# Optimization experiments

Hardware: AMD Instinct MI355X
Metric: run time of the kernel (lower is better)

Reference implementation:

```python
import jax, jax.numpy as jnp
import numpy as np

DIM = 128
CODEBOOK_SIZE = 1024
DECAY = 0.99
EPSILON = 1e-06


def setup_inputs() -> dict:
    key = jax.random.key(0)
    k1, k2, k3, k4 = jax.random.split(key, 4)
    x = jax.random.normal(k1, (64, 1024, DIM), dtype=jnp.float32)
    embed = jax.random.normal(k2, (CODEBOOK_SIZE, DIM), dtype=jnp.float32)
    # keep all codes above the dead-code threshold (2) so expire_codes_ is a no-op
    cluster_size = jax.random.uniform(k3, (CODEBOOK_SIZE,), dtype=jnp.float32) * 10.0 + 2.0
    embed_avg = jax.random.normal(k4, (CODEBOOK_SIZE, DIM), dtype=jnp.float32)
    return {"x": x, "embed": embed, "cluster_size": cluster_size, "embed_avg": embed_avg}


def reference(x, embed, cluster_size, embed_avg):
    shape = x.shape
    xf = x.reshape(-1, shape[-1])  # [N, D]

    # quantize: squared euclidean distances [N, K] then argmin
    dist = (
        jnp.sum(xf * xf, axis=1, keepdims=True)
        - 2.0 * (xf @ embed.T)
        + jnp.sum(embed * embed, axis=1)[None, :]
    )
    embed_ind_flat = jnp.argmin(dist, axis=-1)  # [N]
    embed_ind = embed_ind_flat.reshape(shape[:-1])

    # dequantize
    quantize = embed[embed_ind]  # [..., D]

    # training EMA updates (one-hot scatter accumulation)
    one_hot_sum = jax.ops.segment_sum(
        jnp.ones_like(embed_ind_flat, dtype=x.dtype), embed_ind_flat,
        num_segments=CODEBOOK_SIZE)
    embed_sum = jax.ops.segment_sum(xf, embed_ind_flat, num_segments=CODEBOOK_SIZE)  # [K, D]

    cluster_size_new = cluster_size * DECAY + one_hot_sum * (1.0 - DECAY)
    embed_avg_new = embed_avg * DECAY + embed_sum * (1.0 - DECAY)

    total = jnp.sum(cluster_size_new)
    smoothed = (cluster_size_new + EPSILON) / (total + EPSILON * CODEBOOK_SIZE) * total
    embed_new = embed_avg_new / smoothed[:, None]

    return quantize, embed_ind, cluster_size_new, embed_avg_new, embed_new
```

## Files before the change

kernel.cpp:

```cpp
#include <hip/hip_runtime.h>
#include <hip/hip_fp16.h>
#include <float.h>

#define DIMD   128
#define KCODES 1024
#define NROWS  65536
#define TAU    0.03f
#define SEG_R  16

typedef __attribute__((ext_vector_type(8)))  _Float16 half8;
typedef __attribute__((ext_vector_type(16))) float f32x16;

union U8 { uint4 u; half8 h; };

__device__ __forceinline__ unsigned packh2(float a, float b) {
    __half2 t = __floats2half2_rn(a, b);
    return *(unsigned*)&t;
}

__global__ __launch_bounds__(256) void pre_kernel(
    const float* __restrict__ embed, uint4* __restrict__ ehg,
    float* __restrict__ enorm, uint4* __restrict__ zero_region)
{
    if (blockIdx.x < 64) {
        int t = blockIdx.x * 256 + threadIdx.x;
        int chunk = t >> 9;
        int s = (t >> 6) & 7;
        int L = t & 63;
        const float* src = embed + ((size_t)(chunk * 32 + (L & 31)) * DIMD) + s * 16 + (L >> 5) * 8;
        float4 a = *(const float4*)src;
        float4 b = *(const float4*)(src + 4);
        float f[8] = {a.x, a.y, a.z, a.w, b.x, b.y, b.z, b.w};
        uint4 H;
        unsigned* hw = (unsigned*)&H;
#pragma unroll
        for (int j = 0; j < 4; ++j) hw[j] = packh2(f[2 * j], f[2 * j + 1]);
        ehg[t] = H;
    } else if (blockIdx.x < 68) {
        int k = (blockIdx.x - 64) * 256 + threadIdx.x;
        const float4* e = (const float4*)(embed + (size_t)k * DIMD);
        float s = 0.f;
#pragma unroll
        for (int c = 0; c < DIMD / 4; ++c) {
            float4 v = e[c];
            s += v.x * v.x + v.y * v.y + v.z * v.z + v.w * v.w;
        }
        enorm[k] = s;
    } else {
        uint4 z = {0, 0, 0, 0};
        zero_region[threadIdx.x] = z;
        zero_region[threadIdx.x + 256] = z;
    }
}

__global__ __launch_bounds__(256, 2) void argmin_mfma(
    const float* __restrict__ x, const uint4* __restrict__ ehg,
    const float* __restrict__ enorm,
    int* __restrict__ ind_i, float* __restrict__ ind_f,
    int* __restrict__ wl, int* __restrict__ wl_cnt)
{
    __shared__ uint4 Bs[512];

    const int tid  = threadIdx.x;
    const int wave = tid >> 6;
    const int lane = tid & 63;
    const int n    = lane & 31;
    const int h    = lane >> 5;
    const int row0 = blockIdx.x * 128;
    const int rowA = row0 + wave * 32 + n;

    uint4 xh[8], xl[8];
    const float* xrow = x + (size_t)rowA * DIMD + h * 8;
#pragma unroll
    for (int s = 0; s < 8; ++s) {
        float4 a = *(const float4*)(xrow + s * 16);
        float4 b = *(const float4*)(xrow + s * 16 + 4);
        float f[8] = {a.x, a.y, a.z, a.w, b.x, b.y, b.z, b.w};
        unsigned* ph = (unsigned*)&xh[s];
        unsigned* pl = (unsigned*)&xl[s];
#pragma unroll
        for (int j = 0; j < 4; ++j) {
            float u0 = f[2 * j], u1 = f[2 * j + 1];
            __half2 hh = __floats2half2_rn(u0, u1);
            ph[j] = *(unsigned*)&hh;
            float2 back = __half22float2(hh);
            __half2 ll = __floats2half2_rn(u0 - back.x, u1 - back.y);
            pl[j] = *(unsigned*)&ll;
        }
    }

    float bestv[16], best2[16];
    int   besti[16];
#pragma unroll
    for (int r = 0; r < 16; ++r) { bestv[r] = FLT_MAX; best2[r] = FLT_MAX; besti[r] = 0; }

    for (int chunk = 0; chunk < KCODES / 32; ++chunk) {
        __syncthreads();
        {
            const uint4* sh = ehg + chunk * 512;
            Bs[tid]       = sh[tid];
            Bs[tid + 256] = sh[tid + 256];
        }
        float ee_val = enorm[chunk * 32 + n];
        __syncthreads();

        f32x16 acc;
#pragma unroll
        for (int r = 0; r < 16; ++r) acc[r] = 0.f;

#pragma unroll
        for (int s = 0; s < 8; ++s) {
            U8 ah, al, bh;
            ah.u = xh[s]; al.u = xl[s];
            bh.u = Bs[s * 64 + lane];
            acc = __builtin_amdgcn_mfma_f32_32x32x16_f16(ah.h, bh.h, acc, 0, 0, 0);
            acc = __builtin_amdgcn_mfma_f32_32x32x16_f16(al.h, bh.h, acc, 0, 0, 0);
        }

        const int nglob = chunk * 32 + n;
#pragma unroll
        for (int r = 0; r < 16; ++r) {
            float d = fmaf(-2.f, acc[r], ee_val);
            bool c1 = d < bestv[r];
            float t = c1 ? bestv[r] : d;
            best2[r] = fminf(best2[r], t);
            besti[r] = c1 ? nglob : besti[r];
            bestv[r] = fminf(bestv[r], d);
        }
    }

#pragma unroll
    for (int m = 1; m <= 16; m <<= 1) {
#pragma unroll
        for (int r = 0; r < 16; ++r) {
            float ov = __shfl_xor(bestv[r], m, 64);
            float o2 = __shfl_xor(best2[r], m, 64);
            int   oi = __shfl_xor(besti[r], m, 64);
            float hi = fmaxf(bestv[r], ov);
            best2[r] = fminf(fminf(best2[r], o2), hi);
            bool take = (ov < bestv[r]) || (ov == bestv[r] && oi < besti[r]);
            bestv[r] = take ? ov : bestv[r];
            besti[r] = take ? oi : besti[r];
        }
    }

    if (n == 0) {
#pragma unroll
        for (int r = 0; r < 16; ++r) {
            int row = row0 + wave * 32 + (r & 3) + 8 * (r >> 2) + 4 * h;
            ind_i[row] = besti[r];
            ind_f[row] = (float)besti[r];
            if (best2[r] - bestv[r] < TAU) {
                int p = atomicAdd(wl_cnt, 1);
                if (p < NROWS) wl[p] = row;
            }
        }
    }
}

__global__ __launch_bounds__(256) void recheck_kernel(
    const float* __restrict__ x, const float* __restrict__ embed,
    const float* __restrict__ enorm, const int* __restrict__ wl,
    const int* __restrict__ wl_cnt, int* __restrict__ ind_i, float* __restrict__ ind_f)
{
    __shared__ float xs[DIMD];
    __shared__ float rv[256];
    __shared__ int   ri[256];
    const int tid = threadIdx.x;
    int count = *wl_cnt;
    if (count > NROWS) count = NROWS;

    for (int i = blockIdx.x; i < count; i += gridDim.x) {
        const int row = wl[i];
        __syncthreads();
        if (tid < DIMD) xs[tid] = x[(size_t)row * DIMD + tid];
        __syncthreads();

        const float4* xs4 = (const float4*)xs;
        float xn = 0.f;
#pragma unroll 8
        for (int c = 0; c < 32; ++c) {
            float4 v = xs4[c];
            xn += v.x * v.x + v.y * v.y + v.z * v.z + v.w * v.w;
        }

        float bv = FLT_MAX; int bi = 0;
#pragma unroll
        for (int c = 0; c < 4; ++c) {
            int code = tid * 4 + c;
            const float4* er = (const float4*)(embed + (size_t)code * DIMD);
            float acc = 0.f;
#pragma unroll 8
            for (int kk = 0; kk < 32; ++kk) {
                float4 a = xs4[kk];
                float4 b = er[kk];
                acc += a.x * b.x + a.y * b.y + a.z * b.z + a.w * b.w;
            }
            float d = (xn - 2.0f * acc) + enorm[code];
            if (d < bv) { bv = d; bi = code; }
        }
        rv[tid] = bv; ri[tid] = bi;
        __syncthreads();
        for (int s = 128; s > 0; s >>= 1) {
            if (tid < s) {
                if (rv[tid + s] < rv[tid] || (rv[tid + s] == rv[tid] && ri[tid + s] < ri[tid])) {
                    rv[tid] = rv[tid + s]; ri[tid] = ri[tid + s];
                }
            }
            __syncthreads();
        }
        if (tid == 0) {
            int s_new = ri[0];
            if (s_new != ind_i[row]) {
                ind_i[row] = s_new;
                ind_f[row] = (float)s_new;
            }
        }
        __syncthreads();
    }
}

__global__ __launch_bounds__(256) void hist_kernel(
    const int* __restrict__ ind, int* __restrict__ counts)
{
    __shared__ int hcnt[KCODES];
    for (int i = threadIdx.x; i < KCODES; i += 256) hcnt[i] = 0;
    __syncthreads();
    const int base = blockIdx.x * 2048;
    for (int i = threadIdx.x; i < 2048; i += 256) atomicAdd(&hcnt[ind[base + i]], 1);
    __syncthreads();
    for (int i = threadIdx.x; i < KCODES; i += 256) {
        int v = hcnt[i];
        if (v) atomicAdd(&counts[i], v);
    }
}

__global__ __launch_bounds__(1024) void scan_cluster_kernel(
    const int* __restrict__ counts, const float* __restrict__ cluster_size,
    int* __restrict__ cursor, float* __restrict__ out_cs, float* __restrict__ smoothed)
{
    __shared__ int   s[KCODES];
    __shared__ float rf[KCODES];
    const int t = threadIdx.x;
    int my = counts[t];
    s[t] = my;
    float cs = cluster_size[t] * 0.99f + (float)my * 0.01f;
    out_cs[t] = cs;
    rf[t] = cs;
    __syncthreads();
    for (int d = 1; d < KCODES; d <<= 1) {
        int v = (t >= d) ? s[t - d] : 0;
        __syncthreads();
        s[t] += v;
        __syncthreads();
    }
    cursor[t] = s[t] - my;
    for (int st = 512; st > 0; st >>= 1) {
        if (t < st) rf[t] += rf[t + st];
        __syncthreads();
    }
    float total = rf[0];
    smoothed[t] = (cs + 1e-6f) / (total + 1e-6f * (float)KCODES) * total;
}

__global__ __launch_bounds__(256) void permbuild_kernel(
    const int* __restrict__ ind, int* __restrict__ cursor,
    int* __restrict__ perm, int* __restrict__ codes, uint4* __restrict__ embed_sum4)
{
    const int tid = threadIdx.x;
    if (tid < 128) {
        uint4 z = {0, 0, 0, 0};
        embed_sum4[blockIdx.x * 128 + tid] = z;
    }
    const int row = blockIdx.x * 256 + tid;
    const int k = ind[row];
    int pos = atomicAdd(&cursor[k], 1);
    perm[pos] = row;
    codes[pos] = k;
}

__global__ __launch_bounds__(256) void segsum_kernel(
    const float* __restrict__ x, const float* __restrict__ embed,
    const int* __restrict__ perm, const int* __restrict__ codes,
    float* __restrict__ embed_sum, float* __restrict__ out_q)
{
    const int g = (blockIdx.x * 256 + threadIdx.x) >> 5;
    const int c = threadIdx.x & 31;
    const int base = g * SEG_R;

    float4 acc = {0.f, 0.f, 0.f, 0.f};
    int curk = codes[base];
#pragma unroll
    for (int j = 0; j < SEG_R; ++j) {
        int r = perm[base + j];
        int k = codes[base + j];
        float4 v = *(const float4*)(x + (size_t)r * DIMD + c * 4);
        float4 e = *(const float4*)(embed + (size_t)k * DIMD + c * 4);
        *(float4*)(out_q + (size_t)r * DIMD + c * 4) = e;
        if (k != curk) {
            float* dst = embed_sum + (size_t)curk * DIMD + c * 4;
            atomicAdd(dst + 0, acc.x);
            atomicAdd(dst + 1, acc.y);
            atomicAdd(dst + 2, acc.z);
            atomicAdd(dst + 3, acc.w);
            acc = v;
            curk = k;
        } else {
            acc.x += v.x; acc.y += v.y; acc.z += v.z; acc.w += v.w;
        }
    }
    float* dst = embed_sum + (size_t)curk * DIMD + c * 4;
    atomicAdd(dst + 0, acc.x);
    atomicAdd(dst + 1, acc.y);
    atomicAdd(dst + 2, acc.z);
    atomicAdd(dst + 3, acc.w);
}

__global__ void embed_kernel(
    const float* __restrict__ embed_avg, const float* __restrict__ embed_sum,
    const float* __restrict__ smoothed, float* __restrict__ out_ea,
    float* __restrict__ out_en)
{
    int i = blockIdx.x * blockDim.x + threadIdx.x;
    if (i < KCODES * DIMD) {
        float ea = embed_avg[i] * 0.99f + embed_sum[i] * 0.01f;
        out_ea[i] = ea;
        out_en[i] = ea / smoothed[i >> 7];
    }
}

extern "C" void kernel_launch(void* const* d_in, const int* in_sizes, int n_in,
                              void* d_out, int out_size, void* d_ws, size_t ws_size,
                              hipStream_t stream) {
    const float* x            = (const float*)d_in[0];
    const float* embed        = (const float*)d_in[1];
    const float* cluster_size = (const float*)d_in[2];
    const float* embed_avg    = (const float*)d_in[3];

    float* out     = (float*)d_out;
    float* out_q   = out;
    float* out_ind = out + 8388608;
    float* out_cs  = out + 8454144;
    float* out_ea  = out + 8455168;
    float* out_en  = out + 8586240;

    char* ws = (char*)d_ws;
    int*   ind_i     = (int*)(ws + 0);
    float* enorm     = (float*)(ws + 262144);
    int*   countsI   = (int*)(ws + 266240);
    int*   wl_cnt    = (int*)(ws + 270336);
    int*   cursor    = (int*)(ws + 274432);
    float* smoothed  = (float*)(ws + 278528);
    int*   perm      = (int*)(ws + 286720);
    int*   wl        = (int*)(ws + 548864);
    int*   codes     = (int*)(ws + 548864);
    uint4* ehg       = (uint4*)(ws + 811008);
    float* embed_sum = (float*)(ws + 811008);

    pre_kernel<<<69, 256, 0, stream>>>(embed, ehg, enorm, (uint4*)countsI);
    argmin_mfma<<<NROWS / 128, 256, 0, stream>>>(
        x, ehg, enorm, ind_i, out_ind, wl, wl_cnt);
    recheck_kernel<<<512, 256, 0, stream>>>(
        x, embed, enorm, wl, wl_cnt, ind_i, out_ind);
    hist_kernel<<<32, 256, 0, stream>>>(ind_i, countsI);
    scan_cluster_kernel<<<1, 1024, 0, stream>>>(countsI, cluster_size, cursor, out_cs, smoothed);
    permbuild_kernel<<<NROWS / 256, 256, 0, stream>>>(
        ind_i, cursor, perm, codes, (uint4*)embed_sum);
    segsum_kernel<<<(NROWS / SEG_R) * 32 / 256, 256, 0, stream>>>(
        x, embed, perm, codes, embed_sum, out_q);
    embed_kernel<<<(KCODES * DIMD + 255) / 256, 256, 0, stream>>>(
        embed_avg, embed_sum, smoothed, out_ea, out_en);
}
```

Measured before the change: 240.9 us.

## Double-buffer codebook tiles via direct global-to-LDS loads and pack argmin keys

Codebook chunks are staged into a double-buffered LDS array with global_load_lds, so the next chunk's load overlaps the current chunk's MFMAs and one barrier per iteration is removed. Codebook norms are preloaded into shared memory once per block. The running argmin packs the chunk index into the low mantissa bits of the distance and tracks min and second-min with integer min/max, replacing the float compares and selects. The near-tie threshold is raised slightly to absorb the lost mantissa precision, which sends more rows to recheck. Integer ordering of negative float bit patterns also risks picking the wrong code.

```diff
diff --git a/kernel.cpp b/kernel.cpp
--- a/kernel.cpp
+++ b/kernel.cpp
@@ -5,7 +5,7 @@
 #define DIMD   128
 #define KCODES 1024
 #define NROWS  65536
-#define TAU    0.03f
+#define TAU    0.032f
 #define SEG_R  16
 
 typedef __attribute__((ext_vector_type(8)))  _Float16 half8;
@@ -16,6 +16,12 @@
 __device__ __forceinline__ unsigned packh2(float a, float b) {
     __half2 t = __floats2half2_rn(a, b);
     return *(unsigned*)&t;
+}
+
+__device__ __forceinline__ void stage16(const uint4* g, uint4* l) {
+    auto* gp = (const __attribute__((address_space(1))) uint4*)g;
+    auto* lp = (__attribute__((address_space(3))) uint4*)l;
+    __builtin_amdgcn_global_load_lds(gp, lp, 16, 0, 0);
 }
 
 __global__ __launch_bounds__(256) void pre_kernel(
@@ -59,7 +65,8 @@
     int* __restrict__ ind_i, float* __restrict__ ind_f,
     int* __restrict__ wl, int* __restrict__ wl_cnt)
 {
-    __shared__ uint4 Bs[512];
+    __shared__ uint4 Bs[2][512];
+    __shared__ float Es[KCODES];
 
     const int tid  = threadIdx.x;
     const int wave = tid >> 6;
@@ -69,15 +76,20 @@
     const int row0 = blockIdx.x * 128;
     const int rowA = row0 + wave * 32 + n;
 
-    uint4 xh[8], xl[8];
+    stage16(ehg + tid,       &Bs[0][tid]);
+    stage16(ehg + tid + 256, &Bs[0][tid + 256]);
+    ((float4*)Es)[tid] = ((const float4*)enorm)[tid];
+
+    half8 xh[8], xl[8];
     const float* xrow = x + (size_t)rowA * DIMD + h * 8;
 #pragma unroll
     for (int s = 0; s < 8; ++s) {
         float4 a = *(const float4*)(xrow + s * 16);
         float4 b = *(const float4*)(xrow + s * 16 + 4);
         float f[8] = {a.x, a.y, a.z, a.w, b.x, b.y, b.z, b.w};
-        unsigned* ph = (unsigned*)&xh[s];
-        unsigned* pl = (unsigned*)&xl[s];
+        U8 th, tl;
+        unsigned* ph = (unsigned*)&th.u;
+        unsigned* pl = (unsigned*)&tl.u;
 #pragma unroll
         for (int j = 0; j < 4; ++j) {
             float u0 = f[2 * j], u1 = f[2 * j + 1];
@@ -87,60 +99,69 @@
             __half2 ll = __floats2half2_rn(u0 - back.x, u1 - back.y);
             pl[j] = *(unsigned*)&ll;
         }
-    }
-
-    float bestv[16], best2[16];
-    int   besti[16];
-#pragma unroll
-    for (int r = 0; r < 16; ++r) { bestv[r] = FLT_MAX; best2[r] = FLT_MAX; besti[r] = 0; }
+        xh[s] = th.h; xl[s] = tl.h;
+    }
+
+    int bestv[16], best2[16];
+#pragma unroll
+    for (int r = 0; r < 16; ++r) { bestv[r] = 0x7FFFFFFF; best2[r] = 0x7FFFFFFF; }
 
     for (int chunk = 0; chunk < KCODES / 32; ++chunk) {
-        __syncthreads();
-        {
-            const uint4* sh = ehg + chunk * 512;
-            Bs[tid]       = sh[tid];
-            Bs[tid + 256] = sh[tid + 256];
-        }
-        float ee_val = enorm[chunk * 32 + n];
-        __syncthreads();
+        const int cur = chunk & 1;
+        __syncthreads();
+        if (chunk < KCODES / 32 - 1) {
+            const uint4* gN = ehg + (chunk + 1) * 512;
+            stage16(gN + tid,       &Bs[cur ^ 1][tid]);
+            stage16(gN + tid + 256, &Bs[cur ^ 1][tid + 256]);
+        }
+
+        float ee_val = Es[(chunk << 5) + n];
+
+        const half8* Bh = (const half8*)Bs[cur];
+        half8 bh[8];
+#pragma unroll
+        for (int s = 0; s < 8; ++s) bh[s] = Bh[s * 64 + lane];
 
         f32x16 acc;
 #pragma unroll
         for (int r = 0; r < 16; ++r) acc[r] = 0.f;
-
 #pragma unroll
         for (int s = 0; s < 8; ++s) {
-            U8 ah, al, bh;
-            ah.u = xh[s]; al.u = xl[s];
-            bh.u = Bs[s * 64 + lane];
-            acc = __builtin_amdgcn_mfma_f32_32x32x16_f16(ah.h, bh.h, acc, 0, 0, 0);
-            acc = __builtin_amdgcn_mfma_f32_32x32x16_f16(al.h, bh.h, acc, 0, 0, 0);
-        }
-
-        const int nglob = chunk * 32 + n;
+            acc = __builtin_amdgcn_mfma_f32_32x32x16_f16(xh[s], bh[s], acc, 0, 0, 0);
+            acc = __builtin_amdgcn_mfma_f32_32x32x16_f16(xl[s], bh[s], acc, 0, 0, 0);
+        }
+
 #pragma unroll
         for (int r = 0; r < 16; ++r) {
             float d = fmaf(-2.f, acc[r], ee_val);
-            bool c1 = d < bestv[r];
-            float t = c1 ? bestv[r] : d;
-            best2[r] = fminf(best2[r], t);
-            besti[r] = c1 ? nglob : besti[r];
-            bestv[r] = fminf(bestv[r], d);
-        }
+            int p = (int)((__float_as_int(d) & 0xFFFFFFE0u) | (unsigned)chunk);
+            int old = bestv[r];
+            bestv[r] = min(old, p);
+            best2[r] = min(best2[r], max(old, p));
+        }
+    }
+
+    float fv[16], f2[16];
+    int   bi[16];
+#pragma unroll
+    for (int r = 0; r < 16; ++r) {
+        fv[r] = __int_as_float((int)(bestv[r] & 0xFFFFFFE0u));
+        f2[r] = __int_as_float((int)(best2[r] & 0xFFFFFFE0u));
+        bi[r] = ((bestv[r] & 31) << 5) | n;
     }
 
 #pragma unroll
     for (int m = 1; m <= 16; m <<= 1) {
 #pragma unroll
         for (int r = 0; r < 16; ++r) {
-            float ov = __shfl_xor(bestv[r], m, 64);
-            float o2 = __shfl_xor(best2[r], m, 64);
-            int   oi = __shfl_xor(besti[r], m, 64);
-            float hi = fmaxf(bestv[r], ov);
-            best2[r] = fminf(fminf(best2[r], o2), hi);
-            bool take = (ov < bestv[r]) || (ov == bestv[r] && oi < besti[r]);
-            bestv[r] = take ? ov : bestv[r];
-            besti[r] = take ? oi : besti[r];
+            float ov = __shfl_xor(fv[r], m, 64);
+            float o2 = __shfl_xor(f2[r], m, 64);
+            int   oi = __shfl_xor(bi[r], m, 64);
+            float hi = fmaxf(fv[r], ov);
+            f2[r] = fminf(fminf(f2[r], o2), hi);
+            bool take = (ov < fv[r]) || (ov == fv[r] && oi < bi[r]);
+            fv[r] = take ? ov : fv[r];
+            bi[r] = take ? oi : bi[r];
         }
     }
 
@@ -148,9 +169,9 @@
 #pragma unroll
         for (int r = 0; r < 16; ++r) {
             int row = row0 + wave * 32 + (r & 3) + 8 * (r >> 2) + 4 * h;
-            ind_i[row] = besti[r];
-            ind_f[row] = (float)besti[r];
-            if (best2[r] - bestv[r] < TAU) {
+            ind_i[row] = bi[r];
+            ind_f[row] = (float)bi[r];
+            if (f2[r] - fv[r] < TAU) {
                 int p = atomicAdd(wl_cnt, 1);
                 if (p < NROWS) wl[p] = row;
             }
```

Result: slower. 261.0 us (+8.3%).

## Split dequantize into coalesced kernel and fuse histogram into single-block scan

Applied to the files above, without the earlier changes.

Moves the quantize gather/write out of the permuted segment-sum kernel into a dedicated kernel that writes output rows in natural order, so the stores are coalesced instead of scattered by the permutation. The separate multi-block histogram kernel and its global atomics are merged into the scan kernel, where one 1024-thread block builds the histogram in shared memory. The cost is one block doing all 65536 histogram atomics serially, which may be slower than the 32-block version, and an extra launch for dequantize.

```diff
diff --git a/kernel.cpp b/kernel.cpp
--- a/kernel.cpp
+++ b/kernel.cpp
@@ -220,30 +220,34 @@
     }
 }
 
-__global__ __launch_bounds__(256) void hist_kernel(
-    const int* __restrict__ ind, int* __restrict__ counts)
-{
-    __shared__ int hcnt[KCODES];
-    for (int i = threadIdx.x; i < KCODES; i += 256) hcnt[i] = 0;
-    __syncthreads();
-    const int base = blockIdx.x * 2048;
-    for (int i = threadIdx.x; i < 2048; i += 256) atomicAdd(&hcnt[ind[base + i]], 1);
-    __syncthreads();
-    for (int i = threadIdx.x; i < KCODES; i += 256) {
-        int v = hcnt[i];
-        if (v) atomicAdd(&counts[i], v);
-    }
-}
-
-__global__ __launch_bounds__(1024) void scan_cluster_kernel(
-    const int* __restrict__ counts, const float* __restrict__ cluster_size,
+__global__ __launch_bounds__(256) void dequant_kernel(
+    const int* __restrict__ ind, const float* __restrict__ embed,
+    float* __restrict__ out_q)
+{
+    const int t   = threadIdx.x;
+    const int row = blockIdx.x * 16 + (t >> 4);
+    const int seg = t & 15;
+    const int k   = ind[row];
+    const float4* src = (const float4*)(embed + (size_t)k * DIMD + seg * 8);
+    float4* dst = (float4*)(out_q + (size_t)row * DIMD + seg * 8);
+    dst[0] = src[0];
+    dst[1] = src[1];
+}
+
+__global__ __launch_bounds__(1024) void histscan_kernel(
+    const int* __restrict__ ind, const float* __restrict__ cluster_size,
     int* __restrict__ cursor, float* __restrict__ out_cs, float* __restrict__ smoothed)
 {
     __shared__ int   s[KCODES];
     __shared__ float rf[KCODES];
     const int t = threadIdx.x;
-    int my = counts[t];
-    s[t] = my;
+    s[t] = 0;
+    __syncthreads();
+#pragma unroll
+    for (int i = 0; i < NROWS / 1024; ++i)
+        atomicAdd(&s[ind[i * 1024 + t]], 1);
+    __syncthreads();
+    int my = s[t];
     float cs = cluster_size[t] * 0.99f + (float)my * 0.01f;
     out_cs[t] = cs;
     rf[t] = cs;
@@ -280,9 +284,9 @@
 }
 
 __global__ __launch_bounds__(256) void segsum_kernel(
-    const float* __restrict__ x, const float* __restrict__ embed,
+    const float* __restrict__ x,
     const int* __restrict__ perm, const int* __restrict__ codes,
-    float* __restrict__ embed_sum, float* __restrict__ out_q)
+    float* __restrict__ embed_sum)
 {
     const int g = (blockIdx.x * 256 + threadIdx.x) >> 5;
     const int c = threadIdx.x & 31;
@@ -295,8 +299,6 @@
         int r = perm[base + j];
         int k = codes[base + j];
         float4 v = *(const float4*)(x + (size_t)r * DIMD + c * 4);
-        float4 e = *(const float4*)(embed + (size_t)k * DIMD + c * 4);
-        *(float4*)(out_q + (size_t)r * DIMD + c * 4) = e;
         if (k != curk) {
             float* dst = embed_sum + (size_t)curk * DIMD + c * 4;
             atomicAdd(dst + 0, acc.x);
@@ -362,12 +364,12 @@
         x, ehg, enorm, ind_i, out_ind, wl, wl_cnt);
     recheck_kernel<<<512, 256, 0, stream>>>(
         x, embed, enorm, wl, wl_cnt, ind_i, out_ind);
-    hist_kernel<<<32, 256, 0, stream>>>(ind_i, countsI);
-    scan_cluster_kernel<<<1, 1024, 0, stream>>>(countsI, cluster_size, cursor, out_cs, smoothed);
+    dequant_kernel<<<NROWS / 16, 256, 0, stream>>>(ind_i, embed, out_q);
+    histscan_kernel<<<1, 1024, 0, stream>>>(ind_i, cluster_size, cursor, out_cs, smoothed);
     permbuild_kernel<<<NROWS / 256, 256, 0, stream>>>(
         ind_i, cursor, perm, codes, (uint4*)embed_sum);
     segsum_kernel<<<(NROWS / SEG_R) * 32 / 256, 256, 0, stream>>>(
-        x, embed, perm, codes, embed_sum, out_q);
+        x, perm, codes, embed_sum);
     embed_kernel<<<(KCODES * DIMD + 255) / 256, 256, 0, stream>>>(
         embed_avg, embed_sum, smoothed, out_ea, out_en);
 }
```

Result: slower. 260.8 us (+8.3%).
